# Optimization experiments

Hardware: AMD Instinct MI355X
Metric: run time of the kernel (lower is better)

Reference implementation:

```python
import jax, jax.numpy as jnp
import numpy as np

NUM_USERS = 100000
NUM_ITEMS = 100000
SEQ_LEN = 32
EMBED_DIM = 64
FC_DIM = 100
BATCH = 512
T = 3  # number of target items per example (train mode)


def setup_inputs() -> dict:
    key = jax.random.key(0)
    ks = jax.random.split(key, 12)
    seq_var = jax.random.randint(ks[0], (BATCH, SEQ_LEN), 0, NUM_ITEMS)
    user_var = jax.random.randint(ks[1], (BATCH, 1), 0, NUM_USERS)
    item_var = jax.random.randint(ks[2], (BATCH, T), 0, NUM_ITEMS)
    # Embedding tables, init normal(0, 1/dim) as in the torch module
    item_emb = jax.random.normal(ks[3], (NUM_ITEMS, EMBED_DIM)) * (1.0 / EMBED_DIM)
    user_emb = jax.random.normal(ks[4], (NUM_USERS, EMBED_DIM)) * (1.0 / EMBED_DIM)
    W2 = jax.random.normal(ks[5], (NUM_ITEMS, FC_DIM + EMBED_DIM)) * (1.0 / (FC_DIM + EMBED_DIM))
    b2 = jnp.zeros((NUM_ITEMS, 1))
    # nn.Linear default init: U(-1/sqrt(fan_in), 1/sqrt(fan_in))
    lim1 = 1.0 / np.sqrt(2 * EMBED_DIM)
    W1 = jax.random.uniform(ks[6], (FC_DIM, 2 * EMBED_DIM), minval=-lim1, maxval=lim1)
    b1 = jax.random.uniform(ks[7], (FC_DIM,), minval=-lim1, maxval=lim1)
    lim2 = 1.0 / np.sqrt(FC_DIM)
    Wf2 = jax.random.uniform(ks[8], (FC_DIM, FC_DIM), minval=-lim2, maxval=lim2)
    bf2 = jax.random.uniform(ks[9], (FC_DIM,), minval=-lim2, maxval=lim2)
    return dict(seq_var=seq_var, user_var=user_var, item_var=item_var,
                item_emb=item_emb, user_emb=user_emb, W2=W2, b2=b2,
                W1=W1, b1=b1, Wf2=Wf2, bf2=bf2)


def reference(seq_var, user_var, item_var, item_emb, user_emb, W2, b2, W1, b1, Wf2, bf2):
    # Dropout is identity in eval mode.
    d = item_emb.shape[1]
    embs = item_emb[seq_var]          # [B, L, d]
    uemb = user_emb[user_var]         # [B, 1, d]
    # fc1 on concat(item_i, item_j): split W1 columns so we never build the
    # [B, L, L, 2d] concat tensor; same math as Linear(cat([i, j])).
    Wa, Wb = W1[:, :d], W1[:, d:]     # [FC, d] each
    # all_embed[b, a, c] = cat(embs[b, c], embs[b, a])  (item_i varies with c)
    A = jnp.einsum('bld,fd->blf', embs, Wa)   # applied to item_i (index c)
    Bm = jnp.einsum('bld,fd->blf', embs, Wb)  # applied to item_j (index a)
    h = jax.nn.relu(A[:, None, :, :] + Bm[:, :, None, :] + b1)  # [B, L, L, FC]
    h = jax.nn.relu(jnp.einsum('bacf,gf->bacg', h, Wf2) + bf2)  # [B, L, L, FC]
    x = h.sum((1, 2))                               # [B, FC]
    x = jnp.concatenate([x, uemb[:, 0, :]], axis=1)  # [B, FC + d]
    w2 = W2[item_var]                                # [B, T, FC+d]
    bb = b2[item_var]                                # [B, T, 1]
    out = bb[..., 0] + jnp.einsum('btf,bf->bt', w2, x)  # baddbmm + squeeze -> [B, T]
    return out
```

## Files before the change

kernel.cpp:

```cpp
#include <hip/hip_runtime.h>
#include <hip/hip_bf16.h>

typedef float f32x4 __attribute__((ext_vector_type(4)));
typedef short short8 __attribute__((ext_vector_type(8)));

#define SEQ_LEN 32
#define EMBED_DIM 64
#define FC_DIM 100
#define BATCH 512
#define AS 132
#define ES 80

union FragAB { short8 s; __bf16 h[8]; };

__global__ __launch_bounds__(256, 2) void cosrec_fused(
    const int* __restrict__ seq_var, const int* __restrict__ user_var,
    const int* __restrict__ item_var, const float* __restrict__ item_emb,
    const float* __restrict__ user_emb, const float* __restrict__ W2,
    const float* __restrict__ b2, const float* __restrict__ W1,
    const float* __restrict__ b1, const float* __restrict__ Wf2,
    const float* __restrict__ bf2, float* __restrict__ out)
{
  __shared__ __align__(16) float A_s[SEQ_LEN * AS];
  __shared__ __align__(16) float B_s[SEQ_LEN * AS];
  __shared__ float red_s[16 * 112];
  __shared__ float x_s[112];
  __shared__ __align__(16) __bf16 emb_s[SEQ_LEN * ES];

  const int b = blockIdx.x;
  const int t = threadIdx.x;
  const int w = t >> 6;
  const int l = t & 63;
  const int l15 = l & 15;
  const int q = l >> 4;

  FragAB wfrag[7][4];
  #pragma unroll
  for (int nt = 0; nt < 7; ++nt) {
    const int gg = nt * 16 + l15;
    #pragma unroll
    for (int ks = 0; ks < 4; ++ks) {
      const int f0 = ks * 32 + q * 8;
      if (gg < FC_DIM && ks < 3) {
        const float4 u0 = *(const float4*)(Wf2 + gg * FC_DIM + f0);
        const float4 u1 = *(const float4*)(Wf2 + gg * FC_DIM + f0 + 4);
        wfrag[nt][ks].h[0] = (__bf16)u0.x; wfrag[nt][ks].h[1] = (__bf16)u0.y;
        wfrag[nt][ks].h[2] = (__bf16)u0.z; wfrag[nt][ks].h[3] = (__bf16)u0.w;
        wfrag[nt][ks].h[4] = (__bf16)u1.x; wfrag[nt][ks].h[5] = (__bf16)u1.y;
        wfrag[nt][ks].h[6] = (__bf16)u1.z; wfrag[nt][ks].h[7] = (__bf16)u1.w;
      } else {
        #pragma unroll
        for (int j = 0; j < 8; ++j) {
          const int f = f0 + j;
          wfrag[nt][ks].h[j] = (gg < FC_DIM && f < FC_DIM)
                                   ? (__bf16)Wf2[gg * FC_DIM + f] : (__bf16)0.0f;
        }
      }
    }
  }
  float bf2r[7];
  #pragma unroll
  for (int nt = 0; nt < 7; ++nt) {
    const int gg = nt * 16 + l15;
    bf2r[nt] = (gg < FC_DIM) ? bf2[gg] : 0.0f;
  }

  {
    const int r = t >> 3;
    const int c0 = (t & 7) * 8;
    const int item = seq_var[b * SEQ_LEN + r];
    const float4 v0 = *(const float4*)(item_emb + item * EMBED_DIM + c0);
    const float4 v1 = *(const float4*)(item_emb + item * EMBED_DIM + c0 + 4);
    FragAB e;
    e.h[0] = (__bf16)v0.x; e.h[1] = (__bf16)v0.y;
    e.h[2] = (__bf16)v0.z; e.h[3] = (__bf16)v0.w;
    e.h[4] = (__bf16)v1.x; e.h[5] = (__bf16)v1.y;
    e.h[6] = (__bf16)v1.z; e.h[7] = (__bf16)v1.w;
    *(short8*)(emb_s + r * ES + c0) = e.s;
  }
  for (int i = t; i < SEQ_LEN * 32; i += 256) {
    const int r = i >> 5, c = FC_DIM + (i & 31);
    A_s[r * AS + c] = 0.f;
    B_s[r * AS + c] = 0.f;
  }
  __syncthreads();

  for (int nt = w; nt < 13; nt += 4) {
    const int o = nt * 16 + l15;
    int wr = 0, wc = 0;
    bool valid = true;
    if (o < FC_DIM)            { wr = o;          wc = 0;  }
    else if (o < 2 * FC_DIM)   { wr = o - FC_DIM; wc = 64; }
    else valid = false;
    FragAB bfr[2];
    #pragma unroll
    for (int ks = 0; ks < 2; ++ks) {
      if (valid) {
        const float* p = W1 + wr * 128 + wc + ks * 32 + q * 8;
        const float4 u0 = *(const float4*)p;
        const float4 u1 = *(const float4*)(p + 4);
        bfr[ks].h[0] = (__bf16)u0.x; bfr[ks].h[1] = (__bf16)u0.y;
        bfr[ks].h[2] = (__bf16)u0.z; bfr[ks].h[3] = (__bf16)u0.w;
        bfr[ks].h[4] = (__bf16)u1.x; bfr[ks].h[5] = (__bf16)u1.y;
        bfr[ks].h[6] = (__bf16)u1.z; bfr[ks].h[7] = (__bf16)u1.w;
      } else {
        #pragma unroll
        for (int j = 0; j < 8; ++j) bfr[ks].h[j] = (__bf16)0.0f;
      }
    }
    const float b1v = (o >= FC_DIM && o < 2 * FC_DIM) ? b1[o - FC_DIM] : 0.f;
    #pragma unroll
    for (int mt = 0; mt < 2; ++mt) {
      FragAB afr[2];
      #pragma unroll
      for (int ks = 0; ks < 2; ++ks)
        afr[ks].s = *(const short8*)(emb_s + (mt * 16 + l15) * ES + ks * 32 + q * 8);
      f32x4 acc = {0.f, 0.f, 0.f, 0.f};
      #pragma unroll
      for (int ks = 0; ks < 2; ++ks)
        acc = __builtin_amdgcn_mfma_f32_16x16x32_bf16(afr[ks].s, bfr[ks].s, acc, 0, 0, 0);
      const int row = mt * 16 + q * 4;
      if (o < FC_DIM) {
        #pragma unroll
        for (int r = 0; r < 4; ++r) A_s[(row + r) * AS + o] = acc[r];
      } else if (o < 2 * FC_DIM) {
        #pragma unroll
        for (int r = 0; r < 4; ++r) B_s[(row + r) * AS + (o - FC_DIM)] = acc[r] + b1v;
      }
    }
  }
  __syncthreads();

  float colsum[7];
  #pragma unroll
  for (int nt = 0; nt < 7; ++nt) colsum[nt] = 0.f;

  for (int g = w; g < 8; g += 4) {
    const int c = (g & 1) * 16 + l15;
    const int a0 = (g >> 1) * 8;
    const float4* ap = (const float4*)(A_s + c * AS);
    float areg[32];
    #pragma unroll
    for (int ks = 0; ks < 4; ++ks) {
      const float4 v0 = ap[ks * 8 + q * 2];
      const float4 v1 = ap[ks * 8 + q * 2 + 1];
      areg[ks*8+0] = v0.x; areg[ks*8+1] = v0.y; areg[ks*8+2] = v0.z; areg[ks*8+3] = v0.w;
      areg[ks*8+4] = v1.x; areg[ks*8+5] = v1.y; areg[ks*8+6] = v1.z; areg[ks*8+7] = v1.w;
    }
    for (int ai = 0; ai < 8; ++ai) {
      const float4* bp = (const float4*)(B_s + (a0 + ai) * AS);
      FragAB hf[4];
      #pragma unroll
      for (int ks = 0; ks < 4; ++ks) {
        const float4 b0 = bp[ks * 8 + q * 2];
        const float4 b1f = bp[ks * 8 + q * 2 + 1];
        hf[ks].h[0] = (__bf16)fmaxf(areg[ks*8+0] + b0.x, 0.f);
        hf[ks].h[1] = (__bf16)fmaxf(areg[ks*8+1] + b0.y, 0.f);
        hf[ks].h[2] = (__bf16)fmaxf(areg[ks*8+2] + b0.z, 0.f);
        hf[ks].h[3] = (__bf16)fmaxf(areg[ks*8+3] + b0.w, 0.f);
        hf[ks].h[4] = (__bf16)fmaxf(areg[ks*8+4] + b1f.x, 0.f);
        hf[ks].h[5] = (__bf16)fmaxf(areg[ks*8+5] + b1f.y, 0.f);
        hf[ks].h[6] = (__bf16)fmaxf(areg[ks*8+6] + b1f.z, 0.f);
        hf[ks].h[7] = (__bf16)fmaxf(areg[ks*8+7] + b1f.w, 0.f);
      }
      #pragma unroll
      for (int nt = 0; nt < 7; ++nt) {
        f32x4 acc = {0.f, 0.f, 0.f, 0.f};
        #pragma unroll
        for (int ks = 0; ks < 4; ++ks)
          acc = __builtin_amdgcn_mfma_f32_16x16x32_bf16(hf[ks].s, wfrag[nt][ks].s, acc, 0, 0, 0);
        #pragma unroll
        for (int r = 0; r < 4; ++r)
          colsum[nt] += fmaxf(acc[r] + bf2r[nt], 0.f);
      }
    }
  }

  #pragma unroll
  for (int nt = 0; nt < 7; ++nt)
    red_s[(w * 4 + q) * 112 + nt * 16 + l15] = colsum[nt];
  __syncthreads();
  if (t < 112) {
    float s = 0.f;
    #pragma unroll
    for (int r = 0; r < 16; ++r) s += red_s[r * 112 + t];
    x_s[t] = s;
  }
  __syncthreads();

  float partial = 0.f;
  if (w < 3) {
    const int iv = item_var[b * 3 + w];
    const int uu = user_var[b];
    for (int idx = l; idx < FC_DIM + EMBED_DIM; idx += 64) {
      const float xv = (idx < FC_DIM)
                           ? x_s[idx]
                           : user_emb[uu * EMBED_DIM + (idx - FC_DIM)];
      partial += W2[iv * (FC_DIM + EMBED_DIM) + idx] * xv;
    }
  }
  red_s[w * 64 + l] = partial;
  __syncthreads();
  if (t < 3) {
    float s = 0.f;
    for (int i = 0; i < 64; ++i) s += red_s[t * 64 + i];
    const int iv = item_var[b * 3 + t];
    out[b * 3 + t] = s + b2[iv];
  }
}

extern "C" void kernel_launch(void* const* d_in, const int* in_sizes, int n_in,
                              void* d_out, int out_size, void* d_ws, size_t ws_size,
                              hipStream_t stream) {
  const int* seq = (const int*)d_in[0];
  const int* usr = (const int*)d_in[1];
  const int* itm = (const int*)d_in[2];
  const float* item_emb = (const float*)d_in[3];
  const float* user_emb = (const float*)d_in[4];
  const float* W2  = (const float*)d_in[5];
  const float* b2  = (const float*)d_in[6];
  const float* W1  = (const float*)d_in[7];
  const float* b1  = (const float*)d_in[8];
  const float* Wf2 = (const float*)d_in[9];
  const float* bf2 = (const float*)d_in[10];
  cosrec_fused<<<BATCH, 256, 0, stream>>>(seq, usr, itm, item_emb, user_emb,
                                          W2, b2, W1, b1, Wf2, bf2,
                                          (float*)d_out);
}
```

Before: 160.0 us.

## Switch to fp16 with packed relu and split output tiles into two passes

Stores the fc1 partial sums A and B in shared memory as fp16 rather than fp32. The pairwise add and relu now run as packed half8 vector ops feeding f16 MFMA instead of scalar fp32 adds followed by bf16 conversion. The fc2 weight fragments are no longer held for all 7 output tiles at once: two passes (4 tiles, then 3) each load their own subset, which cuts register pressure but reloads Wf2 and rereads the shared A/B data twice. fp16 changes rounding and range behaviour compared with bf16/fp32.

New measurement: 161.1 us. Within noise of the previous version (+0.7%).

```diff
diff --git a/kernel.cpp b/kernel.cpp
--- a/kernel.cpp
+++ b/kernel.cpp
@@ -1,17 +1,91 @@
 #include <hip/hip_runtime.h>
-#include <hip/hip_bf16.h>
 
 typedef float f32x4 __attribute__((ext_vector_type(4)));
-typedef short short8 __attribute__((ext_vector_type(8)));
+typedef _Float16 half8 __attribute__((ext_vector_type(8)));
 
 #define SEQ_LEN 32
 #define EMBED_DIM 64
 #define FC_DIM 100
 #define BATCH 512
-#define AS 132
-#define ES 80
-
-union FragAB { short8 s; __bf16 h[8]; };
+#define AS2 136
+#define ES 72
+
+union H8 { uint4 u4; half8 v; _Float16 h[8]; };
+
+__device__ __forceinline__ half8 relu8(half8 s) {
+#if __has_builtin(__builtin_elementwise_max)
+  half8 zero = {};
+  return __builtin_elementwise_max(s, zero);
+#else
+  half8 r;
+  #pragma unroll
+  for (int j = 0; j < 8; ++j) r[j] = s[j] > (_Float16)0.f ? s[j] : (_Float16)0.f;
+  return r;
+#endif
+}
+
+template<int NT0, int NT>
+__device__ __forceinline__ void run_pass(
+    const float* __restrict__ Wf2, const float* __restrict__ bf2,
+    const _Float16* A_s2, const _Float16* B_s2,
+    int w, int l15, int q, float* colsum)
+{
+  H8 wfrag[NT][4];
+  float bf2r[NT];
+  #pragma unroll
+  for (int n = 0; n < NT; ++n) {
+    const int gg = (NT0 + n) * 16 + l15;
+    #pragma unroll
+    for (int ks = 0; ks < 4; ++ks) {
+      const int f0 = ks * 32 + q * 8;
+      if (gg < FC_DIM && ks < 3) {
+        const float4 u0 = *(const float4*)(Wf2 + gg * FC_DIM + f0);
+        const float4 u1 = *(const float4*)(Wf2 + gg * FC_DIM + f0 + 4);
+        wfrag[n][ks].h[0] = (_Float16)u0.x; wfrag[n][ks].h[1] = (_Float16)u0.y;
+        wfrag[n][ks].h[2] = (_Float16)u0.z; wfrag[n][ks].h[3] = (_Float16)u0.w;
+        wfrag[n][ks].h[4] = (_Float16)u1.x; wfrag[n][ks].h[5] = (_Float16)u1.y;
+        wfrag[n][ks].h[6] = (_Float16)u1.z; wfrag[n][ks].h[7] = (_Float16)u1.w;
+      } else {
+        #pragma unroll
+        for (int j = 0; j < 8; ++j) {
+          const int f = f0 + j;
+          wfrag[n][ks].h[j] = (gg < FC_DIM && f < FC_DIM)
+                                  ? (_Float16)Wf2[gg * FC_DIM + f] : (_Float16)0.f;
+        }
+      }
+    }
+    bf2r[n] = (gg < FC_DIM) ? bf2[gg] : 0.f;
+  }
+
+  for (int g = w; g < 8; g += 4) {
+    const int c = (g & 1) * 16 + l15;
+    const int a0 = (g >> 1) * 8;
+    H8 areg[4];
+    #pragma unroll
+    for (int ks = 0; ks < 4; ++ks)
+      areg[ks].u4 = *(const uint4*)(A_s2 + c * AS2 + ks * 32 + q * 8);
+    for (int ai = 0; ai < 8; ++ai) {
+      H8 hf[4];
+      #pragma unroll
+      for (int ks = 0; ks < 4; ++ks) {
+        H8 hb;
+        hb.u4 = *(const uint4*)(B_s2 + (a0 + ai) * AS2 + ks * 32 + q * 8);
+        hf[ks].v = relu8(areg[ks].v + hb.v);
+      }
+      #pragma unroll
+      for (int n = 0; n < NT; ++n) {
+        f32x4 acc = {0.f, 0.f, 0.f, 0.f};
+        #pragma unroll
+        for (int ks = 0; ks < 4; ++ks)
+          acc = __builtin_amdgcn_mfma_f32_16x16x32_f16(hf[ks].v, wfrag[n][ks].v,
+                                                       acc, 0, 0, 0);
+        #pragma unroll
+        for (int r = 0; r < 4; ++r)
+          colsum[NT0 + n] += fmaxf(acc[r] + bf2r[n], 0.f);
+      }
+    }
+  }
+}
 
 __global__ __launch_bounds__(256, 2) void cosrec_fused(
     const int* __restrict__ seq_var, const int* __restrict__ user_var,
@@ -21,11 +95,11 @@
     const float* __restrict__ b1, const float* __restrict__ Wf2,
     const float* __restrict__ bf2, float* __restrict__ out)
 {
-  __shared__ __align__(16) float A_s[SEQ_LEN * AS];
-  __shared__ __align__(16) float B_s[SEQ_LEN * AS];
+  __shared__ __align__(16) _Float16 A_s2[SEQ_LEN * AS2];
+  __shared__ __align__(16) _Float16 B_s2[SEQ_LEN * AS2];
+  __shared__ __align__(16) _Float16 emb_s[SEQ_LEN * ES];
   __shared__ float red_s[16 * 112];
   __shared__ float x_s[112];
-  __shared__ __align__(16) __bf16 emb_s[SEQ_LEN * ES];
 
   const int b = blockIdx.x;
   const int t = threadIdx.x;
@@ -34,54 +108,23 @@
   const int l15 = l & 15;
   const int q = l >> 4;
 
-  FragAB wfrag[7][4];
-  #pragma unroll
-  for (int nt = 0; nt < 7; ++nt) {
-    const int gg = nt * 16 + l15;
-    #pragma unroll
-    for (int ks = 0; ks < 4; ++ks) {
-      const int f0 = ks * 32 + q * 8;
-      if (gg < FC_DIM && ks < 3) {
-        const float4 u0 = *(const float4*)(Wf2 + gg * FC_DIM + f0);
-        const float4 u1 = *(const float4*)(Wf2 + gg * FC_DIM + f0 + 4);
-        wfrag[nt][ks].h[0] = (__bf16)u0.x; wfrag[nt][ks].h[1] = (__bf16)u0.y;
-        wfrag[nt][ks].h[2] = (__bf16)u0.z; wfrag[nt][ks].h[3] = (__bf16)u0.w;
-        wfrag[nt][ks].h[4] = (__bf16)u1.x; wfrag[nt][ks].h[5] = (__bf16)u1.y;
-        wfrag[nt][ks].h[6] = (__bf16)u1.z; wfrag[nt][ks].h[7] = (__bf16)u1.w;
-      } else {
-        #pragma unroll
-        for (int j = 0; j < 8; ++j) {
-          const int f = f0 + j;
-          wfrag[nt][ks].h[j] = (gg < FC_DIM && f < FC_DIM)
-                                   ? (__bf16)Wf2[gg * FC_DIM + f] : (__bf16)0.0f;
-        }
-      }
-    }
-  }
-  float bf2r[7];
-  #pragma unroll
-  for (int nt = 0; nt < 7; ++nt) {
-    const int gg = nt * 16 + l15;
-    bf2r[nt] = (gg < FC_DIM) ? bf2[gg] : 0.0f;
-  }
-
   {
     const int r = t >> 3;
     const int c0 = (t & 7) * 8;
     const int item = seq_var[b * SEQ_LEN + r];
     const float4 v0 = *(const float4*)(item_emb + item * EMBED_DIM + c0);
     const float4 v1 = *(const float4*)(item_emb + item * EMBED_DIM + c0 + 4);
-    FragAB e;
-    e.h[0] = (__bf16)v0.x; e.h[1] = (__bf16)v0.y;
-    e.h[2] = (__bf16)v0.z; e.h[3] = (__bf16)v0.w;
-    e.h[4] = (__bf16)v1.x; e.h[5] = (__bf16)v1.y;
-    e.h[6] = (__bf16)v1.z; e.h[7] = (__bf16)v1.w;
-    *(short8*)(emb_s + r * ES + c0) = e.s;
-  }
-  for (int i = t; i < SEQ_LEN * 32; i += 256) {
-    const int r = i >> 5, c = FC_DIM + (i & 31);
-    A_s[r * AS + c] = 0.f;
-    B_s[r * AS + c] = 0.f;
+    H8 e;
+    e.h[0] = (_Float16)v0.x; e.h[1] = (_Float16)v0.y;
+    e.h[2] = (_Float16)v0.z; e.h[3] = (_Float16)v0.w;
+    e.h[4] = (_Float16)v1.x; e.h[5] = (_Float16)v1.y;
+    e.h[6] = (_Float16)v1.z; e.h[7] = (_Float16)v1.w;
+    *(uint4*)(emb_s + r * ES + c0) = e.u4;
+  }
+  for (int i = t; i < SEQ_LEN * 36; i += 256) {
+    const int r = i / 36, c = FC_DIM + (i - r * 36);
+    A_s2[r * AS2 + c] = (_Float16)0.f;
+    B_s2[r * AS2 + c] = (_Float16)0.f;
   }
   __syncthreads();
 
@@ -89,43 +132,45 @@
     const int o = nt * 16 + l15;
     int wr = 0, wc = 0;
     bool valid = true;
-    if (o < FC_DIM)            { wr = o;          wc = 0;  }
-    else if (o < 2 * FC_DIM)   { wr = o - FC_DIM; wc = 64; }
+    if (o < FC_DIM)          { wr = o;          wc = 0;  }
+    else if (o < 2 * FC_DIM) { wr = o - FC_DIM; wc = 64; }
     else valid = false;
-    FragAB bfr[2];
+    H8 bfr[2];
     #pragma unroll
     for (int ks = 0; ks < 2; ++ks) {
       if (valid) {
         const float* p = W1 + wr * 128 + wc + ks * 32 + q * 8;
         const float4 u0 = *(const float4*)p;
         const float4 u1 = *(const float4*)(p + 4);
-        bfr[ks].h[0] = (__bf16)u0.x; bfr[ks].h[1] = (__bf16)u0.y;
-        bfr[ks].h[2] = (__bf16)u0.z; bfr[ks].h[3] = (__bf16)u0.w;
-        bfr[ks].h[4] = (__bf16)u1.x; bfr[ks].h[5] = (__bf16)u1.y;
-        bfr[ks].h[6] = (__bf16)u1.z; bfr[ks].h[7] = (__bf16)u1.w;
+        bfr[ks].h[0] = (_Float16)u0.x; bfr[ks].h[1] = (_Float16)u0.y;
+        bfr[ks].h[2] = (_Float16)u0.z; bfr[ks].h[3] = (_Float16)u0.w;
+        bfr[ks].h[4] = (_Float16)u1.x; bfr[ks].h[5] = (_Float16)u1.y;
+        bfr[ks].h[6] = (_Float16)u1.z; bfr[ks].h[7] = (_Float16)u1.w;
       } else {
         #pragma unroll
-        for (int j = 0; j < 8; ++j) bfr[ks].h[j] = (__bf16)0.0f;
+        for (int j = 0; j < 8; ++j) bfr[ks].h[j] = (_Float16)0.f;
       }
     }
     const float b1v = (o >= FC_DIM && o < 2 * FC_DIM) ? b1[o - FC_DIM] : 0.f;
     #pragma unroll
     for (int mt = 0; mt < 2; ++mt) {
-      FragAB afr[2];
+      H8 afr[2];
       #pragma unroll
       for (int ks = 0; ks < 2; ++ks)
-        afr[ks].s = *(const short8*)(emb_s + (mt * 16 + l15) * ES + ks * 32 + q * 8);
+        afr[ks].u4 = *(const uint4*)(emb_s + (mt * 16 + l15) * ES + ks * 32 + q * 8);
       f32x4 acc = {0.f, 0.f, 0.f, 0.f};
       #pragma unroll
       for (int ks = 0; ks < 2; ++ks)
-        acc = __builtin_amdgcn_mfma_f32_16x16x32_bf16(afr[ks].s, bfr[ks].s, acc, 0, 0, 0);
+        acc = __builtin_amdgcn_mfma_f32_16x16x32_f16(afr[ks].v, bfr[ks].v, acc, 0, 0, 0);
       const int row = mt * 16 + q * 4;
       if (o < FC_DIM) {
         #pragma unroll
-        for (int r = 0; r < 4; ++r) A_s[(row + r) * AS + o] = acc[r];
+        for (int r = 0; r < 4; ++r)
+          A_s2[(row + r) * AS2 + o] = (_Float16)acc[r];
       } else if (o < 2 * FC_DIM) {
         #pragma unroll
-        for (int r = 0; r < 4; ++r) B_s[(row + r) * AS + (o - FC_DIM)] = acc[r] + b1v;
+        for (int r = 0; r < 4; ++r)
+          B_s2[(row + r) * AS2 + (o - FC_DIM)] = (_Float16)(acc[r] + b1v);
       }
     }
   }
@@ -134,47 +179,8 @@
   float colsum[7];
   #pragma unroll
   for (int nt = 0; nt < 7; ++nt) colsum[nt] = 0.f;
-
-  for (int g = w; g < 8; g += 4) {
-    const int c = (g & 1) * 16 + l15;
-    const int a0 = (g >> 1) * 8;
-    const float4* ap = (const float4*)(A_s + c * AS);
-    float areg[32];
-    #pragma unroll
-    for (int ks = 0; ks < 4; ++ks) {
-      const float4 v0 = ap[ks * 8 + q * 2];
-      const float4 v1 = ap[ks * 8 + q * 2 + 1];
-      areg[ks*8+0] = v0.x; areg[ks*8+1] = v0.y; areg[ks*8+2] = v0.z; areg[ks*8+3] = v0.w;
-      areg[ks*8+4] = v1.x; areg[ks*8+5] = v1.y; areg[ks*8+6] = v1.z; areg[ks*8+7] = v1.w;
-    }
-    for (int ai = 0; ai < 8; ++ai) {
-      const float4* bp = (const float4*)(B_s + (a0 + ai) * AS);
-      FragAB hf[4];
-      #pragma unroll
-      for (int ks = 0; ks < 4; ++ks) {
-        const float4 b0 = bp[ks * 8 + q * 2];
-        const float4 b1f = bp[ks * 8 + q * 2 + 1];
-        hf[ks].h[0] = (__bf16)fmaxf(areg[ks*8+0] + b0.x, 0.f);
-        hf[ks].h[1] = (__bf16)fmaxf(areg[ks*8+1] + b0.y, 0.f);
-        hf[ks].h[2] = (__bf16)fmaxf(areg[ks*8+2] + b0.z, 0.f);
-        hf[ks].h[3] = (__bf16)fmaxf(areg[ks*8+3] + b0.w, 0.f);
-        hf[ks].h[4] = (__bf16)fmaxf(areg[ks*8+4] + b1f.x, 0.f);
-        hf[ks].h[5] = (__bf16)fmaxf(areg[ks*8+5] + b1f.y, 0.f);
-        hf[ks].h[6] = (__bf16)fmaxf(areg[ks*8+6] + b1f.z, 0.f);
-        hf[ks].h[7] = (__bf16)fmaxf(areg[ks*8+7] + b1f.w, 0.f);
-      }
-      #pragma unroll
-      for (int nt = 0; nt < 7; ++nt) {
-        f32x4 acc = {0.f, 0.f, 0.f, 0.f};
-        #pragma unroll
-        for (int ks = 0; ks < 4; ++ks)
-          acc = __builtin_amdgcn_mfma_f32_16x16x32_bf16(hf[ks].s, wfrag[nt][ks].s, acc, 0, 0, 0);
-        #pragma unroll
-        for (int r = 0; r < 4; ++r)
-          colsum[nt] += fmaxf(acc[r] + bf2r[nt], 0.f);
-      }
-    }
-  }
+  run_pass<0, 4>(Wf2, bf2, A_s2, B_s2, w, l15, q, colsum);
+  run_pass<4, 3>(Wf2, bf2, A_s2, B_s2, w, l15, q, colsum);
 
   #pragma unroll
   for (int nt = 0; nt < 7; ++nt)
```
